# Kernel optimization log

Hardware: AMD Instinct MI355X
Metric: run time of the kernel (lower is better)

## Reference

```python
import jax, jax.numpy as jnp
import numpy as np

E, N, G = 102400, 100000, 64
D_NODE, D_EDGE, D_GLOB, K = 256, 256, 128, 4
LAYERS = [512, 512, 256]
LN_EPS = 1e-3  # keras LayerNormalization default epsilon


def setup_inputs() -> dict:
    key = jax.random.key(0)
    ks = jax.random.split(key, 12)
    d_in = D_EDGE + K * D_NODE + D_GLOB  # 1408
    inp = {
        "feat": jax.random.normal(ks[0], (E, D_EDGE), jnp.float32),
        "nodes": jax.random.normal(ks[1], (N, D_NODE), jnp.float32),
        "gfeat": jax.random.normal(ks[2], (G, D_GLOB), jnp.float32),
        "ind": jax.random.randint(ks[3], (E, K), 0, N, jnp.int32),
        "num": jnp.full((G,), E // G, jnp.int32),  # sum(num) == E
    }
    dims = [d_in] + LAYERS
    for i in range(3):
        scale = 1.0 / np.sqrt(dims[i])
        inp[f"W{i+1}"] = jax.random.normal(ks[4 + i], (dims[i], dims[i + 1]), jnp.float32) * scale
        inp[f"b{i+1}"] = jnp.zeros((dims[i + 1],), jnp.float32)
    inp["gamma"] = jnp.ones((LAYERS[-1],), jnp.float32)
    inp["beta"] = jnp.zeros((LAYERS[-1],), jnp.float32)
    return inp


def reference(feat, nodes, gfeat, ind, num, W1, b1, W2, b2, W3, b3, gamma, beta):
    e = feat.shape[0]
    # _fixed_number_to_one: gather K nodes per hyperedge, flatten -> [E, K*D_NODE]
    gathered = nodes[ind].reshape(e, -1)
    # _one_to_segments: broadcast per-graph globals to their edges -> [E, D_GLOB]
    graph_ids = jnp.repeat(jnp.arange(num.shape[0]), num, total_repeat_length=e)
    glob = gfeat[graph_ids]
    x = jnp.concatenate([feat, gathered, glob], axis=1)  # [E, 1408]
    h = jax.nn.relu(x @ W1 + b1)
    h = jax.nn.relu(h @ W2 + b2)
    h = jax.nn.sigmoid(h @ W3 + b3)
    # keras LayerNormalization over the last axis
    mu = jnp.mean(h, axis=-1, keepdims=True)
    var = jnp.var(h, axis=-1, keepdims=True)
    return gamma * (h - mu) * jax.lax.rsqrt(var + LN_EPS) + beta
```

## Files before the change

kernel.cpp:

```cpp
#include <hip/hip_runtime.h>
#include <hip/hip_fp16.h>

#define E_EDGES 102400
#define N_NODES 100000
#define G_GRAPHS 64
#define D_EDGE 256
#define D_NODE 256
#define D_GLOB 128
#define KNB 4
#define D_IN 1408
#define H1D 512
#define H2D 512
#define H3D 256
#define LN_EPS 1e-3f

typedef _Float16 half8 __attribute__((ext_vector_type(8)));
typedef float f32x4 __attribute__((ext_vector_type(4)));

__device__ __forceinline__ void gload16(const void* g, void* l) {
    __builtin_amdgcn_global_load_lds((const __attribute__((address_space(1))) void*)g,
                                     (__attribute__((address_space(3))) void*)l, 16, 0, 0);
}


__global__ void k_prefix(const int* __restrict__ num, int* __restrict__ prefix) {
    if (threadIdx.x == 0) {
        int acc = 0;
        prefix[0] = 0;
        for (int g = 0; g < G_GRAPHS; ++g) { acc += num[g]; prefix[g + 1] = acc; }
    }
}

__global__ void k_gid(const int* __restrict__ prefix, int* __restrict__ gid) {
    int e = blockIdx.x * blockDim.x + threadIdx.x;
    if (e >= E_EDGES) return;
    int lo = 0, hi = G_GRAPHS;
    while (hi - lo > 1) {
        int mid = (lo + hi) >> 1;
        if (e >= prefix[mid]) lo = mid; else hi = mid;
    }
    gid[e] = lo;
}

__global__ void k_transpose(const float* __restrict__ src, _Float16* __restrict__ dst,
                            int Ks, int Ns) {
    long total = (long)Ks * Ns;
    for (long idx = (long)blockIdx.x * blockDim.x + threadIdx.x; idx < total;
         idx += (long)gridDim.x * blockDim.x) {
        int n = (int)(idx / Ks);
        int k = (int)(idx - (long)n * Ks);
        dst[idx] = (_Float16)src[(long)k * Ns + n];
    }
}


__global__ void k_gather(const float* __restrict__ feat, const float* __restrict__ nodes,
                         const float* __restrict__ gfeat, const int* __restrict__ ind,
                         const int* __restrict__ gid, _Float16* __restrict__ X) {
    const long total = (long)E_EDGES * (D_IN / 8);
    for (long c = (long)blockIdx.x * blockDim.x + threadIdx.x; c < total;
         c += (long)gridDim.x * blockDim.x) {
        int e = (int)(c / (D_IN / 8));
        int f0 = ((int)(c - (long)e * (D_IN / 8))) * 8;
        const float* s;
        if (f0 < D_EDGE) {
            s = feat + (size_t)e * D_EDGE + f0;
        } else if (f0 < D_EDGE + KNB * D_NODE) {
            int r = f0 - D_EDGE;
            s = nodes + (size_t)ind[e * KNB + (r >> 8)] * D_NODE + (r & 255);
        } else {
            s = gfeat + (size_t)gid[e] * D_GLOB + (f0 - (D_EDGE + KNB * D_NODE));
        }
        float4 u = reinterpret_cast<const float4*>(s)[0];
        float4 v = reinterpret_cast<const float4*>(s)[1];
        half8 h;
        h[0] = (_Float16)u.x; h[1] = (_Float16)u.y; h[2] = (_Float16)u.z; h[3] = (_Float16)u.w;
        h[4] = (_Float16)v.x; h[5] = (_Float16)v.y; h[6] = (_Float16)v.z; h[7] = (_Float16)v.w;
        *reinterpret_cast<half8*>(X + (size_t)e * D_IN + f0) = h;
    }
}


template <int KD>
__global__ __launch_bounds__(256) void k_gemm_relu(
    const _Float16* __restrict__ A, const _Float16* __restrict__ Wt,
    const float* __restrict__ bias, _Float16* __restrict__ out) {
    __shared__ __align__(16) _Float16 As[128][64];
    __shared__ __align__(16) _Float16 Bs[128][64];
    const int t = threadIdx.x;
    const int bn = blockIdx.x, bm = blockIdx.y;
    const int w = t >> 6, lane = t & 63;
    const int wr = w >> 1, wc = w & 1, lr = lane & 15, lk = lane >> 4;
    const int n0 = bn * 128;

    const int srow = w * 8 + (lane >> 3);
    const int scol = (lane & 7) * 8;
    const _Float16* Ab = A + (size_t)(bm * 128 + srow) * KD + scol;
    const _Float16* Bb = Wt + (size_t)(n0 + srow) * KD + scol;

    f32x4 acc[4][4];
#pragma unroll
    for (int m = 0; m < 4; m++)
#pragma unroll
        for (int n = 0; n < 4; n++) acc[m][n] = (f32x4)0.f;

    for (int kt = 0; kt < KD / 64; ++kt) {
        const int k0 = kt * 64;
        __syncthreads();
#pragma unroll
        for (int i = 0; i < 4; i++) {
            gload16(Ab + (size_t)i * 32 * KD + k0, (char*)As + i * 4096 + w * 1024);
            gload16(Bb + (size_t)i * 32 * KD + k0, (char*)Bs + i * 4096 + w * 1024);
        }
        __syncthreads();
#pragma unroll
        for (int kk = 0; kk < 2; kk++) {
            half8 a[4], b[4];
#pragma unroll
            for (int m = 0; m < 4; m++)
                a[m] = *reinterpret_cast<half8*>(&As[wr * 64 + m * 16 + lr][kk * 32 + lk * 8]);
#pragma unroll
            for (int n = 0; n < 4; n++)
                b[n] = *reinterpret_cast<half8*>(&Bs[wc * 64 + n * 16 + lr][kk * 32 + lk * 8]);
#pragma unroll
            for (int m = 0; m < 4; m++)
#pragma unroll
                for (int n = 0; n < 4; n++)
                    acc[m][n] = __builtin_amdgcn_mfma_f32_16x16x32_f16(a[m], b[n], acc[m][n], 0, 0, 0);
        }
    }
#pragma unroll
    for (int n = 0; n < 4; n++) {
        int col = n0 + wc * 64 + n * 16 + lr;
        float bv = bias[col];
#pragma unroll
        for (int m = 0; m < 4; m++) {
            int rbase = bm * 128 + wr * 64 + m * 16 + lk * 4;
#pragma unroll
            for (int q = 0; q < 4; q++) {
                float v = acc[m][n][q] + bv;
                v = v > 0.f ? v : 0.f;
                out[(size_t)(rbase + q) * H1D + col] = (_Float16)v;
            }
        }
    }
}


__global__ __launch_bounds__(512) void k_gemm3_ln(
    const _Float16* __restrict__ A, const _Float16* __restrict__ Wt,
    const float* __restrict__ bias, const float* __restrict__ gamma,
    const float* __restrict__ beta, float* __restrict__ out) {
    __shared__ __align__(16) _Float16 As[128][64];
    __shared__ __align__(16) _Float16 Bs[256][64];
    __shared__ float red1[128][4];
    __shared__ float red2[128][4];
    __shared__ float mvmu[128];
    __shared__ float mvrs[128];
    const int t = threadIdx.x;
    const int bm = blockIdx.x;
    const int w = t >> 6, lane = t & 63;
    const int wr = w >> 2, wc = w & 3, lr = lane & 15, lk = lane >> 4;

    const int srow = w * 8 + (lane >> 3);
    const int scol = (lane & 7) * 8;
    const _Float16* Ab = A + (size_t)(bm * 128 + srow) * H2D + scol;
    const _Float16* Bb = Wt + (size_t)srow * H2D + scol;

    f32x4 acc[4][4];
#pragma unroll
    for (int m = 0; m < 4; m++)
#pragma unroll
        for (int n = 0; n < 4; n++) acc[m][n] = (f32x4)0.f;

    for (int kt = 0; kt < 8; ++kt) {
        const int k0 = kt * 64;
        __syncthreads();
#pragma unroll
        for (int i = 0; i < 2; i++)
            gload16(Ab + (size_t)i * 64 * H2D + k0, (char*)As + i * 8192 + w * 1024);
#pragma unroll
        for (int i = 0; i < 4; i++)
            gload16(Bb + (size_t)i * 64 * H2D + k0, (char*)Bs + i * 8192 + w * 1024);
        __syncthreads();
#pragma unroll
        for (int kk = 0; kk < 2; kk++) {
            half8 a[4], b[4];
#pragma unroll
            for (int m = 0; m < 4; m++)
                a[m] = *reinterpret_cast<half8*>(&As[wr * 64 + m * 16 + lr][kk * 32 + lk * 8]);
#pragma unroll
            for (int n = 0; n < 4; n++)
                b[n] = *reinterpret_cast<half8*>(&Bs[wc * 64 + n * 16 + lr][kk * 32 + lk * 8]);
#pragma unroll
            for (int m = 0; m < 4; m++)
#pragma unroll
                for (int n = 0; n < 4; n++)
                    acc[m][n] = __builtin_amdgcn_mfma_f32_16x16x32_f16(a[m], b[n], acc[m][n], 0, 0, 0);
        }
    }

#pragma unroll
    for (int n = 0; n < 4; n++) {
        int col = wc * 64 + n * 16 + lr;
        float bv = bias[col];
#pragma unroll
        for (int m = 0; m < 4; m++)
#pragma unroll
            for (int q = 0; q < 4; q++) {
                float x = acc[m][n][q] + bv;
                acc[m][n][q] = 1.f / (1.f + __expf(-x));
            }
    }

#pragma unroll
    for (int m = 0; m < 4; m++)
#pragma unroll
        for (int q = 0; q < 4; q++) {
            float s1 = 0.f, s2 = 0.f;
#pragma unroll
            for (int n = 0; n < 4; n++) {
                float x = acc[m][n][q];
                s1 += x; s2 += x * x;
            }
            s1 += __shfl_xor(s1, 1); s2 += __shfl_xor(s2, 1);
            s1 += __shfl_xor(s1, 2); s2 += __shfl_xor(s2, 2);
            s1 += __shfl_xor(s1, 4); s2 += __shfl_xor(s2, 4);
            s1 += __shfl_xor(s1, 8); s2 += __shfl_xor(s2, 8);
            if (lr == 0) {
                int row = wr * 64 + m * 16 + lk * 4 + q;
                red1[row][wc] = s1;
                red2[row][wc] = s2;
            }
        }
    __syncthreads();
    if (t < 128) {
        float s = red1[t][0] + red1[t][1] + red1[t][2] + red1[t][3];
        float ss = red2[t][0] + red2[t][1] + red2[t][2] + red2[t][3];
        float mu = s * (1.f / H3D);
        float var = ss * (1.f / H3D) - mu * mu;
        mvmu[t] = mu;
        mvrs[t] = rsqrtf(var + LN_EPS);
    }
    __syncthreads();
#pragma unroll
    for (int m = 0; m < 4; m++)
#pragma unroll
        for (int q = 0; q < 4; q++) {
            int row = wr * 64 + m * 16 + lk * 4 + q;
            float mu = mvmu[row], rs = mvrs[row];
#pragma unroll
            for (int n = 0; n < 4; n++) {
                int col = wc * 64 + n * 16 + lr;
                out[(size_t)(bm * 128 + row) * H3D + col] =
                    gamma[col] * (acc[m][n][q] - mu) * rs + beta[col];
            }
        }
}


extern "C" void kernel_launch(void* const* d_in, const int* in_sizes, int n_in,
                              void* d_out, int out_size, void* d_ws, size_t ws_size,
                              hipStream_t stream) {
    const float* feat  = (const float*)d_in[0];
    const float* nodes = (const float*)d_in[1];
    const float* gfeat = (const float*)d_in[2];
    const int*   ind   = (const int*)d_in[3];
    const int*   num   = (const int*)d_in[4];
    const float* W1    = (const float*)d_in[5];
    const float* b1    = (const float*)d_in[6];
    const float* W2    = (const float*)d_in[7];
    const float* b2    = (const float*)d_in[8];
    const float* W3    = (const float*)d_in[9];
    const float* b3    = (const float*)d_in[10];
    const float* gamma = (const float*)d_in[11];
    const float* beta  = (const float*)d_in[12];
    float* out = (float*)d_out;

    char* ws = (char*)d_ws;
    size_t off = 0;
    auto alloc = [&](size_t bytes) {
        size_t o = off;
        off += (bytes + 255) & ~(size_t)255;
        return o;
    };
    int* prefix    = (int*)(ws + alloc((G_GRAPHS + 1) * sizeof(int)));
    int* gid       = (int*)(ws + alloc((size_t)E_EDGES * sizeof(int)));
    _Float16* W1t  = (_Float16*)(ws + alloc((size_t)H1D * D_IN * 2));
    _Float16* W2t  = (_Float16*)(ws + alloc((size_t)H2D * H1D * 2));
    _Float16* W3t  = (_Float16*)(ws + alloc((size_t)H3D * H2D * 2));
    _Float16* X    = (_Float16*)(ws + alloc((size_t)E_EDGES * D_IN * 2));
    _Float16* h1   = (_Float16*)(ws + alloc((size_t)E_EDGES * H1D * 2));
    _Float16* h2   = X;
    (void)ws_size; (void)in_sizes; (void)n_in; (void)out_size;

    k_prefix<<<1, 64, 0, stream>>>(num, prefix);
    k_gid<<<(E_EDGES + 255) / 256, 256, 0, stream>>>(prefix, gid);
    k_transpose<<<1024, 256, 0, stream>>>(W1, W1t, D_IN, H1D);
    k_transpose<<<512, 256, 0, stream>>>(W2, W2t, H1D, H2D);
    k_transpose<<<256, 256, 0, stream>>>(W3, W3t, H2D, H3D);
    k_gather<<<2048, 256, 0, stream>>>(feat, nodes, gfeat, ind, gid, X);
    k_gemm_relu<D_IN><<<dim3(H1D / 128, E_EDGES / 128), 256, 0, stream>>>(X, W1t, b1, h1);
    k_gemm_relu<H1D><<<dim3(H2D / 128, E_EDGES / 128), 256, 0, stream>>>(h1, W2t, b2, h2);
    k_gemm3_ln<<<E_EDGES / 128, 512, 0, stream>>>(h2, W3t, b3, gamma, beta, out);
}
```

Baseline: 737.3 us.

## Fuse gather into first GEMM with triple-buffered swizzled 128x256 pipeline

Removes the materialized X gather buffer. Feat, nodes and gfeat are pre-converted to fp16, and the first GEMM loads A tiles directly from the gathered rows. Both ReLU GEMMs move to a 512-thread 128x256 tile with a three-stage LDS ring buffer (144KB), async global_load_lds prefetch two tiles ahead, XOR-swizzled LDS layout to avoid bank conflicts, and setprio around the MFMA blocks. This cuts the large X write and read-back traffic and overlaps loads with compute. The cost is extra conversion passes over nodes/feat, the large LDS footprint limiting occupancy to one block per CU, and a separate h2 buffer.

```diff
diff --git a/kernel.cpp b/kernel.cpp
--- a/kernel.cpp
+++ b/kernel.cpp
@@ -53,50 +53,52 @@
     }
 }
 
-
-__global__ void k_gather(const float* __restrict__ feat, const float* __restrict__ nodes,
-                         const float* __restrict__ gfeat, const int* __restrict__ ind,
-                         const int* __restrict__ gid, _Float16* __restrict__ X) {
-    const long total = (long)E_EDGES * (D_IN / 8);
-    for (long c = (long)blockIdx.x * blockDim.x + threadIdx.x; c < total;
-         c += (long)gridDim.x * blockDim.x) {
-        int e = (int)(c / (D_IN / 8));
-        int f0 = ((int)(c - (long)e * (D_IN / 8))) * 8;
-        const float* s;
-        if (f0 < D_EDGE) {
-            s = feat + (size_t)e * D_EDGE + f0;
-        } else if (f0 < D_EDGE + KNB * D_NODE) {
-            int r = f0 - D_EDGE;
-            s = nodes + (size_t)ind[e * KNB + (r >> 8)] * D_NODE + (r & 255);
-        } else {
-            s = gfeat + (size_t)gid[e] * D_GLOB + (f0 - (D_EDGE + KNB * D_NODE));
-        }
-        float4 u = reinterpret_cast<const float4*>(s)[0];
-        float4 v = reinterpret_cast<const float4*>(s)[1];
+__global__ void k_cvt16(const float* __restrict__ src, _Float16* __restrict__ dst, long n8) {
+    for (long i = (long)blockIdx.x * blockDim.x + threadIdx.x; i < n8;
+         i += (long)gridDim.x * blockDim.x) {
+        float4 u = reinterpret_cast<const float4*>(src)[i * 2];
+        float4 v = reinterpret_cast<const float4*>(src)[i * 2 + 1];
         half8 h;
         h[0] = (_Float16)u.x; h[1] = (_Float16)u.y; h[2] = (_Float16)u.z; h[3] = (_Float16)u.w;
         h[4] = (_Float16)v.x; h[5] = (_Float16)v.y; h[6] = (_Float16)v.z; h[7] = (_Float16)v.w;
-        *reinterpret_cast<half8*>(X + (size_t)e * D_IN + f0) = h;
-    }
-}
-
-
-template <int KD>
-__global__ __launch_bounds__(256) void k_gemm_relu(
-    const _Float16* __restrict__ A, const _Float16* __restrict__ Wt,
+        reinterpret_cast<half8*>(dst)[i] = h;
+    }
+}
+
+
+template <int KD, bool GATHER>
+__global__ __launch_bounds__(512) void k_gemm_pipe(
+    const _Float16* __restrict__ A,
+    const _Float16* __restrict__ feat16, const _Float16* __restrict__ nodes16,
+    const _Float16* __restrict__ gfeat16,
+    const int* __restrict__ ind, const int* __restrict__ gid,
+    const _Float16* __restrict__ Wt,
     const float* __restrict__ bias, _Float16* __restrict__ out) {
-    __shared__ __align__(16) _Float16 As[128][64];
-    __shared__ __align__(16) _Float16 Bs[128][64];
+    constexpr int NT = KD / 64;
+    __shared__ __align__(16) char lds[3 * 49152];
+
     const int t = threadIdx.x;
     const int bn = blockIdx.x, bm = blockIdx.y;
+    const int n0 = bn * 256;
     const int w = t >> 6, lane = t & 63;
-    const int wr = w >> 1, wc = w & 1, lr = lane & 15, lk = lane >> 4;
-    const int n0 = bn * 128;
-
-    const int srow = w * 8 + (lane >> 3);
-    const int scol = (lane & 7) * 8;
-    const _Float16* Ab = A + (size_t)(bm * 128 + srow) * KD + scol;
-    const _Float16* Bb = Wt + (size_t)(n0 + srow) * KD + scol;
+    const int wr = w >> 2, wc = w & 3;
+    const int lr = lane & 15, lk = lane >> 4;
+
+    const int srow = t >> 3;
+    const int gslot = (t & 7) ^ (srow & 7);
+    const int wbase = w * 8;
+
+    int4 iv0, iv1;
+    int g0 = 0, g1 = 0;
+    int e0 = 0, e1 = 0;
+    if constexpr (GATHER) {
+        e0 = bm * 128 + srow;
+        e1 = e0 + 64;
+        iv0 = *reinterpret_cast<const int4*>(ind + (size_t)e0 * KNB);
+        iv1 = *reinterpret_cast<const int4*>(ind + (size_t)e1 * KNB);
+        g0 = gid[e0];
+        g1 = gid[e1];
+    }
 
     f32x4 acc[4][4];
 #pragma unroll
@@ -104,40 +106,85 @@
 #pragma unroll
         for (int n = 0; n < 4; n++) acc[m][n] = (f32x4)0.f;
 
-    for (int kt = 0; kt < KD / 64; ++kt) {
-        const int k0 = kt * 64;
-        __syncthreads();
-#pragma unroll
-        for (int i = 0; i < 4; i++) {
-            gload16(Ab + (size_t)i * 32 * KD + k0, (char*)As + i * 4096 + w * 1024);
-            gload16(Bb + (size_t)i * 32 * KD + k0, (char*)Bs + i * 4096 + w * 1024);
-        }
-        __syncthreads();
-#pragma unroll
-        for (int kk = 0; kk < 2; kk++) {
+    auto stage = [&](int kt, char* abuf, char* bbuf) {
+#pragma unroll
+        for (int c = 0; c < 2; ++c) {
+            const _Float16* src;
+            if constexpr (GATHER) {
+                if (kt < 4) {
+                    src = feat16 + (size_t)(c ? e1 : e0) * D_EDGE + kt * 64;
+                } else if (kt < 20) {
+                    int j = (kt - 4) >> 2;
+                    int4 iv = c ? iv1 : iv0;
+                    int nidx = j == 0 ? iv.x : j == 1 ? iv.y : j == 2 ? iv.z : iv.w;
+                    src = nodes16 + (size_t)nidx * D_NODE + ((kt - 4) & 3) * 64;
+                } else {
+                    src = gfeat16 + (size_t)(c ? g1 : g0) * D_GLOB + (kt - 20) * 64;
+                }
+            } else {
+                src = A + (size_t)(bm * 128 + c * 64 + srow) * KD + kt * 64;
+            }
+            gload16(src + gslot * 8, abuf + (c * 64 + wbase) * 128);
+        }
+#pragma unroll
+        for (int c = 0; c < 4; ++c) {
+            const _Float16* src = Wt + (size_t)(n0 + c * 64 + srow) * KD + kt * 64;
+            gload16(src + gslot * 8, bbuf + (c * 64 + wbase) * 128);
+        }
+    };
+
+    stage(0, lds, lds + 16384);
+    stage(1, lds + 49152, lds + 49152 + 16384);
+    asm volatile("s_waitcnt vmcnt(6)" ::: "memory");
+    __builtin_amdgcn_s_barrier();
+
+    int cur = 0;
+    for (int kt = 0; kt < NT; ++kt) {
+        const int pf = kt + 2;
+        if (pf < NT) {
+            const int pb = cur == 0 ? 2 : cur - 1;
+            stage(pf, lds + pb * 49152, lds + pb * 49152 + 16384);
+        }
+        const char* ab = lds + cur * 49152;
+        const char* bb = ab + 16384;
+#pragma unroll
+        for (int kk = 0; kk < 2; ++kk) {
             half8 a[4], b[4];
 #pragma unroll
-            for (int m = 0; m < 4; m++)
-                a[m] = *reinterpret_cast<half8*>(&As[wr * 64 + m * 16 + lr][kk * 32 + lk * 8]);
-#pragma unroll
-            for (int n = 0; n < 4; n++)
-                b[n] = *reinterpret_cast<half8*>(&Bs[wc * 64 + n * 16 + lr][kk * 32 + lk * 8]);
-#pragma unroll
-            for (int m = 0; m < 4; m++)
-#pragma unroll
-                for (int n = 0; n < 4; n++)
+            for (int m = 0; m < 4; ++m) {
+                int row = wr * 64 + m * 16 + lr;
+                a[m] = *reinterpret_cast<const half8*>(
+                    ab + row * 128 + ((((kk << 2) | lk)) ^ (lr & 7)) * 16);
+            }
+#pragma unroll
+            for (int n = 0; n < 4; ++n) {
+                int row = wc * 64 + n * 16 + lr;
+                b[n] = *reinterpret_cast<const half8*>(
+                    bb + row * 128 + ((((kk << 2) | lk)) ^ (lr & 7)) * 16);
+            }
+            __builtin_amdgcn_s_setprio(1);
+#pragma unroll
+            for (int m = 0; m < 4; ++m)
+#pragma unroll
+                for (int n = 0; n < 4; ++n)
                     acc[m][n] = __builtin_amdgcn_mfma_f32_16x16x32_f16(a[m], b[n], acc[m][n], 0, 0, 0);
-        }
-    }
-#pragma unroll
-    for (int n = 0; n < 4; n++) {
+            __builtin_amdgcn_s_setprio(0);
+        }
+        if (pf < NT) asm volatile("s_waitcnt vmcnt(6)" ::: "memory");
+        else         asm volatile("s_waitcnt vmcnt(0)" ::: "memory");
+        __builtin_amdgcn_s_barrier();
+        cur = cur == 2 ? 0 : cur + 1;
+    }
+
+#pragma unroll
+    for (int n = 0; n < 4; ++n) {
         int col = n0 + wc * 64 + n * 16 + lr;
         float bv = bias[col];
 #pragma unroll
-        for (int m = 0; m < 4; m++) {
+        for (int m = 0; m < 4; ++m) {
             int rbase = bm * 128 + wr * 64 + m * 16 + lk * 4;
 #pragma unroll
-            for (int q = 0; q < 4; q++) {
+            for (int q = 0; q < 4; ++q) {
                 float v = acc[m][n][q] + bv;
                 v = v > 0.f ? v : 0.f;
                 out[(size_t)(rbase + q) * H1D + col] = (_Float16)v;
@@ -284,23 +331,29 @@
         off += (bytes + 255) & ~(size_t)255;
         return o;
     };
-    int* prefix    = (int*)(ws + alloc((G_GRAPHS + 1) * sizeof(int)));
-    int* gid       = (int*)(ws + alloc((size_t)E_EDGES * sizeof(int)));
-    _Float16* W1t  = (_Float16*)(ws + alloc((size_t)H1D * D_IN * 2));
-    _Float16* W2t  = (_Float16*)(ws + alloc((size_t)H2D * H1D * 2));
-    _Float16* W3t  = (_Float16*)(ws + alloc((size_t)H3D * H2D * 2));
-    _Float16* X    = (_Float16*)(ws + alloc((size_t)E_EDGES * D_IN * 2));
-    _Float16* h1   = (_Float16*)(ws + alloc((size_t)E_EDGES * H1D * 2));
-    _Float16* h2   = X;
+    int* prefix       = (int*)(ws + alloc((G_GRAPHS + 1) * sizeof(int)));
+    int* gid          = (int*)(ws + alloc((size_t)E_EDGES * sizeof(int)));
+    _Float16* W1t     = (_Float16*)(ws + alloc((size_t)H1D * D_IN * 2));
+    _Float16* W2t     = (_Float16*)(ws + alloc((size_t)H2D * H1D * 2));
+    _Float16* W3t     = (_Float16*)(ws + alloc((size_t)H3D * H2D * 2));
+    _Float16* feat16  = (_Float16*)(ws + alloc((size_t)E_EDGES * D_EDGE * 2));
+    _Float16* nodes16 = (_Float16*)(ws + alloc((size_t)N_NODES * D_NODE * 2));
+    _Float16* gfeat16 = (_Float16*)(ws + alloc((size_t)G_GRAPHS * D_GLOB * 2));
+    _Float16* h1      = (_Float16*)(ws + alloc((size_t)E_EDGES * H1D * 2));
+    _Float16* h2      = (_Float16*)(ws + alloc((size_t)E_EDGES * H2D * 2));
     (void)ws_size; (void)in_sizes; (void)n_in; (void)out_size;
 
     k_prefix<<<1, 64, 0, stream>>>(num, prefix);
     k_gid<<<(E_EDGES + 255) / 256, 256, 0, stream>>>(prefix, gid);
+    k_cvt16<<<2048, 256, 0, stream>>>(feat, feat16, (long)E_EDGES * D_EDGE / 8);
+    k_cvt16<<<2048, 256, 0, stream>>>(nodes, nodes16, (long)N_NODES * D_NODE / 8);
+    k_cvt16<<<16, 256, 0, stream>>>(gfeat, gfeat16, (long)G_GRAPHS * D_GLOB / 8);
     k_transpose<<<1024, 256, 0, stream>>>(W1, W1t, D_IN, H1D);
     k_transpose<<<512, 256, 0, stream>>>(W2, W2t, H1D, H2D);
     k_transpose<<<256, 256, 0, stream>>>(W3, W3t, H2D, H3D);
-    k_gather<<<2048, 256, 0, stream>>>(feat, nodes, gfeat, ind, gid, X);
-    k_gemm_relu<D_IN><<<dim3(H1D / 128, E_EDGES / 128), 256, 0, stream>>>(X, W1t, b1, h1);
-    k_gemm_relu<H1D><<<dim3(H2D / 128, E_EDGES / 128), 256, 0, stream>>>(h1, W2t, b2, h2);
+    k_gemm_pipe<D_IN, true><<<dim3(H1D / 256, E_EDGES / 128), 512, 0, stream>>>(
+        nullptr, feat16, nodes16, gfeat16, ind, gid, W1t, b1, h1);
+    k_gemm_pipe<H1D, false><<<dim3(H2D / 256, E_EDGES / 128), 512, 0, stream>>>(
+        h1, nullptr, nullptr, nullptr, nullptr, nullptr, W2t, b2, h2);
     k_gemm3_ln<<<E_EDGES / 128, 512, 0, stream>>>(h2, W3t, b3, gamma, beta, out);
 }
```

New measurement: 629.9 us. -14.6%, faster.
